# Performance work log

Hardware: AMD Instinct MI355X
Metric: run time of the kernel (lower is better)

Reference implementation:

```python
import jax, jax.numpy as jnp
import numpy as np

ALPHA = 0.2  # LeakyReLU negative slope


def setup_inputs() -> dict:
    key = jax.random.key(0)
    k_x, k_w, k_a = jax.random.split(key, 3)
    B, N, F_in = 4, 2048, 128
    H, nhid = 4, 32  # out_channel=128, nheads=4
    x = jax.random.normal(k_x, (B, N, F_in), dtype=jnp.float32)
    # per-head projection and attention vector, xavier-ish scale
    W = jax.random.normal(k_w, (H, F_in, nhid), dtype=jnp.float32) * (1.414 * np.sqrt(2.0 / (F_in + nhid))) / np.sqrt(3.0) * np.sqrt(3.0)
    a = jax.random.normal(k_a, (H, 2 * nhid), dtype=jnp.float32) * (1.414 * np.sqrt(2.0 / (2 * nhid + 1)))
    return {"x": x, "W": W, "a": a}


def reference(x, W, a):
    # x: [B,N,F_in], W: [H,F_in,d], a: [H,2d]
    H = W.shape[0]
    d = W.shape[2]
    B, N, _ = x.shape
    Wh = jnp.einsum('bni,hij->bhnj', x, W)          # [B,H,N,d]
    a1 = a[:, :d]                                    # [H,d]
    a2 = a[:, d:]                                    # [H,d]
    Wh1 = jnp.einsum('bhnd,hd->bhn', Wh, a1)         # [B,H,N]
    Wh2 = jnp.einsum('bhnd,hd->bhn', Wh, a2)         # [B,H,N]
    e = Wh1[:, :, :, None] + Wh2[:, :, None, :]      # [B,H,N,N]
    e = jnp.where(e > 0, e, ALPHA * e)               # LeakyReLU
    attn = jax.nn.softmax(e, axis=-1)                # softmax over source nodes
    h = jnp.einsum('bhij,bhjd->bhid', attn, Wh)      # [B,H,N,d]
    h = jax.nn.elu(h)
    # concat heads along feature dim: [B,N,H*d]
    out = jnp.transpose(h, (0, 2, 1, 3)).reshape(B, N, H * d)
    return out
```

## Files before the change

### kernel.cpp

```cpp
#include <hip/hip_runtime.h>


#define LOG2E 1.4426950408889634f
constexpr int Nn = 2048, Fin = 128, Dd = 32;

typedef _Float16 half8 __attribute__((ext_vector_type(8)));
typedef _Float16 half4v __attribute__((ext_vector_type(4)));
typedef _Float16 half2v __attribute__((ext_vector_type(2)));
typedef float f32x4 __attribute__((ext_vector_type(4)));

union H8 { half2v h2[4]; half8 h8; };

__global__ __launch_bounds__(256) void k1_wh(
    const float* __restrict__ x, const float* __restrict__ W,
    const float* __restrict__ a, _Float16* __restrict__ whT,
    float* __restrict__ sArr, float* __restrict__ tArr) {
  constexpr int KLD = 136;
  __shared__ __align__(16) _Float16 Wlds[2 * 32 * KLD];
  _Float16* BhL = Wlds;
  _Float16* BlL = Wlds + 32 * KLD;

  int blk = blockIdx.x;
  int bh = blk >> 5, tile = blk & 31;
  int b = bh >> 2, h = bh & 3;
  int tid = threadIdx.x, w = tid >> 6, lane = tid & 63;
  int q = lane >> 4, m = lane & 15;
  int rowbase = tile * 64 + w * 16;

  const float* Wq = W + h * Fin * Dd;
  {
    int k = tid >> 1, dbase = (tid & 1) * 16;
    const float* wp = Wq + k * Dd + dbase;
    float4 w0 = *(const float4*)(wp);
    float4 w1 = *(const float4*)(wp + 4);
    float4 w2 = *(const float4*)(wp + 8);
    float4 w3 = *(const float4*)(wp + 12);
    float wv[16] = {w0.x, w0.y, w0.z, w0.w, w1.x, w1.y, w1.z, w1.w,
                    w2.x, w2.y, w2.z, w2.w, w3.x, w3.y, w3.z, w3.w};
#pragma unroll
    for (int u = 0; u < 16; ++u) {
      _Float16 hi = (_Float16)wv[u];
      BhL[(dbase + u) * KLD + k] = hi;
      BlL[(dbase + u) * KLD + k] = (_Float16)(wv[u] - (float)hi);
    }
  }
  __syncthreads();

  const float* xb = x + (size_t)(b * Nn + rowbase + m) * Fin;
  f32x4 acc[2];
  acc[0] = (f32x4){0.f, 0.f, 0.f, 0.f};
  acc[1] = (f32x4){0.f, 0.f, 0.f, 0.f};

#pragma unroll
  for (int kt = 0; kt < 4; ++kt) {
    float4 x0 = *(const float4*)(xb + kt * 32 + q * 8);
    float4 x1 = *(const float4*)(xb + kt * 32 + q * 8 + 4);
    float xv[8] = {x0.x, x0.y, x0.z, x0.w, x1.x, x1.y, x1.z, x1.w};
    half8 Ah, Al;
#pragma unroll
    for (int j = 0; j < 8; ++j) {
      _Float16 hi = (_Float16)xv[j];
      Ah[j] = hi;
      Al[j] = (_Float16)(xv[j] - (float)hi);
    }
#pragma unroll
    for (int nt = 0; nt < 2; ++nt) {
      int off = (nt * 16 + m) * KLD + kt * 32 + q * 8;
      half8 Bh = *(const half8*)&BhL[off];
      half8 Bl = *(const half8*)&BlL[off];
      acc[nt] = __builtin_amdgcn_mfma_f32_16x16x32_f16(Ah, Bh, acc[nt], 0, 0, 0);
      acc[nt] = __builtin_amdgcn_mfma_f32_16x16x32_f16(Al, Bh, acc[nt], 0, 0, 0);
      acc[nt] = __builtin_amdgcn_mfma_f32_16x16x32_f16(Ah, Bl, acc[nt], 0, 0, 0);
    }
  }

#pragma unroll
  for (int nt = 0; nt < 2; ++nt) {
    int d = nt * 16 + m;
    half4v h4;
#pragma unroll
    for (int r = 0; r < 4; ++r) h4[r] = (_Float16)acc[nt][r];
    *(half4v*)(whT + (size_t)(bh * Dd + d) * Nn + rowbase + q * 4) = h4;
  }

  const float* ah = a + h * 2 * Dd;
  float a1m0 = ah[m], a1m1 = ah[16 + m];
  float a2m0 = ah[Dd + m], a2m1 = ah[Dd + 16 + m];
#pragma unroll
  for (int r = 0; r < 4; ++r) {
    float ps = acc[0][r] * a1m0 + acc[1][r] * a1m1;
    float pt = acc[0][r] * a2m0 + acc[1][r] * a2m1;
#pragma unroll
    for (int off = 1; off < 16; off <<= 1) {
      ps += __shfl_xor(ps, off);
      pt += __shfl_xor(pt, off);
    }
    if (m == 0) {
      sArr[bh * Nn + rowbase + q * 4 + r] = ps;
      tArr[bh * Nn + rowbase + q * 4 + r] = pt;
    }
  }
}

__global__ __launch_bounds__(256) void k3_attn(
    const _Float16* __restrict__ whT, const float* __restrict__ sArr,
    const float* __restrict__ tArr, float* __restrict__ out) {
  __shared__ float smem[4 * 64 * 33 + 256];
  _Float16* Ef = (_Float16*)smem;
  _Float16* Ff = (_Float16*)(smem + 1024);
  float* red = smem + 2048;

  int blk = blockIdx.x;
  int bh = blk >> 5, tile = blk & 31;
  int b = bh >> 2, h = bh & 3;
  int tid = threadIdx.x, w = tid >> 6, lane = tid & 63;
  int q = lane >> 4, m = lane & 15;

  float tv[8];
  float mx = -1e30f;
#pragma unroll
  for (int k = 0; k < 8; ++k) {
    tv[k] = tArr[bh * Nn + tid + k * 256];
    mx = fmaxf(mx, tv[k]);
  }
  red[tid] = mx;
  __syncthreads();
  for (int ss = 128; ss > 0; ss >>= 1) {
    if (tid < ss) red[tid] = fmaxf(red[tid], red[tid + ss]);
    __syncthreads();
  }
  float T = red[0];
  __syncthreads();
#pragma unroll
  for (int k = 0; k < 8; ++k) {
    float dt = tv[k] - T;
    Ef[tid + k * 256] = (_Float16)__builtin_amdgcn_exp2f(LOG2E * dt);
    Ff[tid + k * 256] = (_Float16)__builtin_amdgcn_exp2f(0.2f * LOG2E * dt);
  }

  half2v aa[4], bb[4];
#pragma unroll
  for (int t = 0; t < 4; ++t) {
    float es = sArr[bh * Nn + tile * 64 + t * 16 + m] + T;
    float al = __builtin_amdgcn_exp2f(0.8f * LOG2E * fminf(es, 0.f));
    float be = __builtin_amdgcn_exp2f(-0.8f * LOG2E * fmaxf(es, 0.f));
    _Float16 ah_ = (_Float16)al, bh_ = (_Float16)be;
    aa[t] = (half2v){ah_, ah_};
    bb[t] = (half2v){bh_, bh_};
  }
  __syncthreads();

  f32x4 acc[4][2];
  f32x4 accd[4];
#pragma unroll
  for (int t = 0; t < 4; ++t) {
    acc[t][0] = (f32x4){0.f, 0.f, 0.f, 0.f};
    acc[t][1] = (f32x4){0.f, 0.f, 0.f, 0.f};
    accd[t] = (f32x4){0.f, 0.f, 0.f, 0.f};
  }
  half8 bden;
  {
    _Float16 v = (_Float16)((m == 0) ? 1.f : 0.f);
#pragma unroll
    for (int j = 0; j < 8; ++j) bden[j] = v;
  }

  const _Float16* wb = whT + (size_t)bh * Dd * Nn;
  const int jb0 = w * 512;

  half8 B0 = *(const half8*)(wb + (size_t)m * Nn + jb0 + q * 8);
  half8 B1 = *(const half8*)(wb + (size_t)(16 + m) * Nn + jb0 + q * 8);
  H8 E, F;
  E.h8 = *(const half8*)&Ef[jb0 + q * 8];
  F.h8 = *(const half8*)&Ff[jb0 + q * 8];

#pragma unroll 2
  for (int s = 0; s < 16; ++s) {
    int jn = jb0 + ((s + 1) & 15) * 32;
    half8 nB0 = *(const half8*)(wb + (size_t)m * Nn + jn + q * 8);
    half8 nB1 = *(const half8*)(wb + (size_t)(16 + m) * Nn + jn + q * 8);
    H8 nE, nF;
    nE.h8 = *(const half8*)&Ef[jn + q * 8];
    nF.h8 = *(const half8*)&Ff[jn + q * 8];

#pragma unroll
    for (int t = 0; t < 4; ++t) {
      H8 P;
#pragma unroll
      for (int kk = 0; kk < 4; ++kk) {
        half2v pe = aa[t] * E.h2[kk];
        half2v pf = bb[t] * F.h2[kk];
        P.h2[kk] = __builtin_elementwise_max(pe, pf);
      }
      acc[t][0] = __builtin_amdgcn_mfma_f32_16x16x32_f16(P.h8, B0, acc[t][0], 0, 0, 0);
      acc[t][1] = __builtin_amdgcn_mfma_f32_16x16x32_f16(P.h8, B1, acc[t][1], 0, 0, 0);
      accd[t]  = __builtin_amdgcn_mfma_f32_16x16x32_f16(P.h8, bden, accd[t], 0, 0, 0);
    }
    B0 = nB0; B1 = nB1; E = nE; F = nF;
  }

  __syncthreads();
  float* redN = smem;
  float* redD = smem + 4 * 64 * 33;
#pragma unroll
  for (int t = 0; t < 4; ++t) {
#pragma unroll
    for (int dh = 0; dh < 2; ++dh)
#pragma unroll
      for (int r = 0; r < 4; ++r)
        redN[(w * 64 + t * 16 + q * 4 + r) * 33 + dh * 16 + m] = acc[t][dh][r];
    if (m == 0) {
#pragma unroll
      for (int r = 0; r < 4; ++r)
        redD[w * 64 + t * 16 + q * 4 + r] = accd[t][r];
    }
  }
  __syncthreads();
  {
    int rl = tid >> 2, dg = (tid & 3) * 8;
    float num[8];
#pragma unroll
    for (int i = 0; i < 8; ++i)
      num[i] = redN[(0 * 64 + rl) * 33 + dg + i] + redN[(1 * 64 + rl) * 33 + dg + i] +
               redN[(2 * 64 + rl) * 33 + dg + i] + redN[(3 * 64 + rl) * 33 + dg + i];
    float dt = redD[rl] + redD[64 + rl] + redD[128 + rl] + redD[192 + rl];
    float rd = 1.0f / dt;
    float* orow = out + (size_t)(b * Nn + tile * 64 + rl) * (4 * Dd) + h * Dd + dg;
#pragma unroll
    for (int i = 0; i < 8; ++i) {
      float hv = num[i] * rd;
      num[i] = hv > 0.f ? hv : (__builtin_amdgcn_exp2f(hv * LOG2E) - 1.0f);
    }
    *(float4*)orow = make_float4(num[0], num[1], num[2], num[3]);
    *((float4*)orow + 1) = make_float4(num[4], num[5], num[6], num[7]);
  }
}

extern "C" void kernel_launch(void* const* d_in, const int* in_sizes, int n_in,
                              void* d_out, int out_size, void* d_ws, size_t ws_size,
                              hipStream_t stream) {
  const float* x = (const float*)d_in[0];
  const float* W = (const float*)d_in[1];
  const float* a = (const float*)d_in[2];
  float* out = (float*)d_out;

  float* wsf = (float*)d_ws;
  float* sArr = wsf;
  float* tArr = sArr + 32768;
  _Float16* whT = (_Float16*)(tArr + 32768);

  k1_wh<<<dim3(512), dim3(256), 0, stream>>>(x, W, a, whT, sArr, tArr);
  k3_attn<<<dim3(512), dim3(256), 0, stream>>>(whT, sArr, tArr, out);
}
```

Baseline: 76.43 us.

## Split attention work across 8 waves by row group and source half

```diff
diff --git a/kernel.cpp b/kernel.cpp
--- a/kernel.cpp
+++ b/kernel.cpp
@@ -102,10 +102,10 @@
   }
 }
 
-__global__ __launch_bounds__(256) void k3_attn(
+__global__ __launch_bounds__(512, 4) void k3_attn(
     const _Float16* __restrict__ whT, const float* __restrict__ sArr,
     const float* __restrict__ tArr, float* __restrict__ out) {
-  __shared__ float smem[4 * 64 * 33 + 256];
+  __shared__ float smem[4352];
   _Float16* Ef = (_Float16*)smem;
   _Float16* Ff = (_Float16*)(smem + 1024);
   float* red = smem + 2048;
@@ -115,49 +115,42 @@
   int b = bh >> 2, h = bh & 3;
   int tid = threadIdx.x, w = tid >> 6, lane = tid & 63;
   int q = lane >> 4, m = lane & 15;
-
-  float tv[8];
+  int wrg = w & 3, wj = w >> 2;
+
+  float tv[4];
   float mx = -1e30f;
 #pragma unroll
-  for (int k = 0; k < 8; ++k) {
-    tv[k] = tArr[bh * Nn + tid + k * 256];
+  for (int k = 0; k < 4; ++k) {
+    tv[k] = tArr[bh * Nn + tid + k * 512];
     mx = fmaxf(mx, tv[k]);
   }
-  red[tid] = mx;
-  __syncthreads();
-  for (int ss = 128; ss > 0; ss >>= 1) {
-    if (tid < ss) red[tid] = fmaxf(red[tid], red[tid + ss]);
-    __syncthreads();
-  }
-  float T = red[0];
-  __syncthreads();
-#pragma unroll
-  for (int k = 0; k < 8; ++k) {
+#pragma unroll
+  for (int off = 32; off > 0; off >>= 1) mx = fmaxf(mx, __shfl_xor(mx, off));
+  if (lane == 0) red[w] = mx;
+  __syncthreads();
+  float T = fmaxf(fmaxf(fmaxf(red[0], red[1]), fmaxf(red[2], red[3])),
+                  fmaxf(fmaxf(red[4], red[5]), fmaxf(red[6], red[7])));
+#pragma unroll
+  for (int k = 0; k < 4; ++k) {
     float dt = tv[k] - T;
-    Ef[tid + k * 256] = (_Float16)__builtin_amdgcn_exp2f(LOG2E * dt);
-    Ff[tid + k * 256] = (_Float16)__builtin_amdgcn_exp2f(0.2f * LOG2E * dt);
-  }
-
-  half2v aa[4], bb[4];
-#pragma unroll
-  for (int t = 0; t < 4; ++t) {
-    float es = sArr[bh * Nn + tile * 64 + t * 16 + m] + T;
+    Ef[tid + k * 512] = (_Float16)__builtin_amdgcn_exp2f(LOG2E * dt);
+    Ff[tid + k * 512] = (_Float16)__builtin_amdgcn_exp2f(0.2f * LOG2E * dt);
+  }
+
+  half2v aa, bb;
+  {
+    float es = sArr[bh * Nn + tile * 64 + wrg * 16 + m] + T;
     float al = __builtin_amdgcn_exp2f(0.8f * LOG2E * fminf(es, 0.f));
     float be = __builtin_amdgcn_exp2f(-0.8f * LOG2E * fmaxf(es, 0.f));
     _Float16 ah_ = (_Float16)al, bh_ = (_Float16)be;
-    aa[t] = (half2v){ah_, ah_};
-    bb[t] = (half2v){bh_, bh_};
-  }
-  __syncthreads();
-
-  f32x4 acc[4][2];
-  f32x4 accd[4];
-#pragma unroll
-  for (int t = 0; t < 4; ++t) {
-    acc[t][0] = (f32x4){0.f, 0.f, 0.f, 0.f};
-    acc[t][1] = (f32x4){0.f, 0.f, 0.f, 0.f};
-    accd[t] = (f32x4){0.f, 0.f, 0.f, 0.f};
-  }
+    aa = (half2v){ah_, ah_};
+    bb = (half2v){bh_, bh_};
+  }
+  __syncthreads();
+
+  f32x4 acc0 = (f32x4){0.f, 0.f, 0.f, 0.f};
+  f32x4 acc1 = (f32x4){0.f, 0.f, 0.f, 0.f};
+  f32x4 accd = (f32x4){0.f, 0.f, 0.f, 0.f};
   half8 bden;
   {
     _Float16 v = (_Float16)((m == 0) ? 1.f : 0.f);
@@ -166,7 +159,7 @@
   }
 
   const _Float16* wb = whT + (size_t)bh * Dd * Nn;
-  const int jb0 = w * 512;
+  const int jb0 = wj * 1024;
 
   half8 B0 = *(const half8*)(wb + (size_t)m * Nn + jb0 + q * 8);
   half8 B1 = *(const half8*)(wb + (size_t)(16 + m) * Nn + jb0 + q * 8);
@@ -175,64 +168,61 @@
   F.h8 = *(const half8*)&Ff[jb0 + q * 8];
 
 #pragma unroll 2
-  for (int s = 0; s < 16; ++s) {
-    int jn = jb0 + ((s + 1) & 15) * 32;
+  for (int s = 0; s < 32; ++s) {
+    int jn = jb0 + ((s + 1) & 31) * 32;
     half8 nB0 = *(const half8*)(wb + (size_t)m * Nn + jn + q * 8);
     half8 nB1 = *(const half8*)(wb + (size_t)(16 + m) * Nn + jn + q * 8);
     H8 nE, nF;
     nE.h8 = *(const half8*)&Ef[jn + q * 8];
     nF.h8 = *(const half8*)&Ff[jn + q * 8];
 
-#pragma unroll
-    for (int t = 0; t < 4; ++t) {
-      H8 P;
-#pragma unroll
-      for (int kk = 0; kk < 4; ++kk) {
-        half2v pe = aa[t] * E.h2[kk];
-        half2v pf = bb[t] * F.h2[kk];
-        P.h2[kk] = __builtin_elementwise_max(pe, pf);
-      }
-      acc[t][0] = __builtin_amdgcn_mfma_f32_16x16x32_f16(P.h8, B0, acc[t][0], 0, 0, 0);
-      acc[t][1] = __builtin_amdgcn_mfma_f32_16x16x32_f16(P.h8, B1, acc[t][1], 0, 0, 0);
-      accd[t]  = __builtin_amdgcn_mfma_f32_16x16x32_f16(P.h8, bden, accd[t], 0, 0, 0);
-    }
+    H8 P;
+#pragma unroll
+    for (int kk = 0; kk < 4; ++kk) {
+      half2v pe = aa * E.h2[kk];
+      half2v pf = bb * F.h2[kk];
+      P.h2[kk] = __builtin_elementwise_max(pe, pf);
+    }
+    acc0 = __builtin_amdgcn_mfma_f32_16x16x32_f16(P.h8, B0, acc0, 0, 0, 0);
+    acc1 = __builtin_amdgcn_mfma_f32_16x16x32_f16(P.h8, B1, acc1, 0, 0, 0);
+    accd = __builtin_amdgcn_mfma_f32_16x16x32_f16(P.h8, bden, accd, 0, 0, 0);
+
     B0 = nB0; B1 = nB1; E = nE; F = nF;
   }
 
   __syncthreads();
   float* redN = smem;
-  float* redD = smem + 4 * 64 * 33;
-#pragma unroll
-  for (int t = 0; t < 4; ++t) {
-#pragma unroll
-    for (int dh = 0; dh < 2; ++dh)
+  float* redD = smem + 4224;
+  {
+    int row = wrg * 16 + q * 4;
+#pragma unroll
+    for (int dh = 0; dh < 2; ++dh) {
+      f32x4 v = dh ? acc1 : acc0;
 #pragma unroll
       for (int r = 0; r < 4; ++r)
-        redN[(w * 64 + t * 16 + q * 4 + r) * 33 + dh * 16 + m] = acc[t][dh][r];
+        redN[(wj * 64 + row + r) * 33 + dh * 16 + m] = v[r];
+    }
     if (m == 0) {
 #pragma unroll
-      for (int r = 0; r < 4; ++r)
-        redD[w * 64 + t * 16 + q * 4 + r] = accd[t][r];
-    }
-  }
-  __syncthreads();
-  {
-    int rl = tid >> 2, dg = (tid & 3) * 8;
-    float num[8];
-#pragma unroll
-    for (int i = 0; i < 8; ++i)
-      num[i] = redN[(0 * 64 + rl) * 33 + dg + i] + redN[(1 * 64 + rl) * 33 + dg + i] +
-               redN[(2 * 64 + rl) * 33 + dg + i] + redN[(3 * 64 + rl) * 33 + dg + i];
-    float dt = redD[rl] + redD[64 + rl] + redD[128 + rl] + redD[192 + rl];
+      for (int r = 0; r < 4; ++r) redD[wj * 64 + row + r] = accd[r];
+    }
+  }
+  __syncthreads();
+  {
+    int rl = tid >> 3, dg = (tid & 7) * 4;
+    float num[4];
+#pragma unroll
+    for (int i = 0; i < 4; ++i)
+      num[i] = redN[rl * 33 + dg + i] + redN[(64 + rl) * 33 + dg + i];
+    float dt = redD[rl] + redD[64 + rl];
     float rd = 1.0f / dt;
     float* orow = out + (size_t)(b * Nn + tile * 64 + rl) * (4 * Dd) + h * Dd + dg;
 #pragma unroll
-    for (int i = 0; i < 8; ++i) {
+    for (int i = 0; i < 4; ++i) {
       float hv = num[i] * rd;
       num[i] = hv > 0.f ? hv : (__builtin_amdgcn_exp2f(hv * LOG2E) - 1.0f);
     }
     *(float4*)orow = make_float4(num[0], num[1], num[2], num[3]);
-    *((float4*)orow + 1) = make_float4(num[4], num[5], num[6], num[7]);
   }
 }
 
@@ -250,5 +240,5 @@
   _Float16* whT = (_Float16*)(tArr + 32768);
 
   k1_wh<<<dim3(512), dim3(256), 0, stream>>>(x, W, a, whT, sArr, tArr);
-  k3_attn<<<dim3(512), dim3(256), 0, stream>>>(whT, sArr, tArr, out);
+  k3_attn<<<dim3(512), dim3(512), 0, stream>>>(whT, sArr, tArr, out);
 }
```

Result: slower. 95.14 us (+24.5%).
